# Kernel tuning notes

Hardware: AMD Instinct MI355X
Metric: run time of the kernel (lower is better)

## Reference

```python
import jax, jax.numpy as jnp
import numpy as np

EPS = 1e-6

def _silu(x):
    return x * jax.nn.sigmoid(x)

def setup_inputs() -> dict:
    key = jax.random.key(0)
    ks = jax.random.split(key, 6)
    T, B, D, N = 2048, 16, 1024, 64
    scale = (6.0 / (N + D)) ** 0.5  # xavier_uniform bound
    x = jax.random.normal(ks[0], (T, B, D), dtype=jnp.float32)
    S0 = jnp.zeros((B, N, N), dtype=jnp.float32)
    W_k = jax.random.uniform(ks[1], (N, D), minval=-scale, maxval=scale, dtype=jnp.float32)
    W_v = jax.random.uniform(ks[2], (N, D), minval=-scale, maxval=scale, dtype=jnp.float32)
    W_q = jax.random.uniform(ks[3], (N, D), minval=-scale, maxval=scale, dtype=jnp.float32)
    W_beta = jax.random.uniform(ks[4], (N, D), minval=-scale, maxval=scale, dtype=jnp.float32)
    b_beta = jnp.full((N,), 2.0, dtype=jnp.float32)
    return {"x": x, "S0": S0, "W_k": W_k, "W_v": W_v, "W_q": W_q, "W_beta": W_beta, "b_beta": b_beta}

def reference(x, S0, W_k, W_v, W_q, W_beta, b_beta):
    # x: [T, B, D] -> projections [T, B, n]
    k_all = jnp.einsum('tbd,nd->tbn', x, W_k)
    v_all = jnp.einsum('tbd,nd->tbn', x, W_v)
    q_all = jnp.einsum('tbd,nd->tbn', x, W_q)
    beta_all = jax.nn.sigmoid(jnp.einsum('tbd,nd->tbn', x, W_beta) + b_beta)

    def step(S, inp):
        k, v, q, beta = inp  # each [B, n]
        k_norm = k / (jnp.linalg.norm(k, axis=-1, keepdims=True) + EPS)
        retrieved = jnp.einsum('bij,bj->bi', S, k_norm)
        delta = v - retrieved
        outer = jnp.einsum('bi,bj->bij', delta, k_norm)
        S_new = jnp.tanh(beta[:, :, None] * S + outer)
        Sq = jnp.einsum('bij,bj->bi', S_new, q)
        out = Sq * _silu(Sq)
        return S_new, out

    S_final, output = jax.lax.scan(step, S0, (k_all, v_all, q_all, beta_all))
    return output, S_final
```

## Files before the change

### kernel.cpp

```cpp
#include <hip/hip_runtime.h>
#include <math.h>
#include <stdint.h>

#define T_DIM 2048
#define B_DIM 16
#define D_DIM 1024
#define N_DIM 64
#define EPSV 1e-6f

#define NT 256

#define TWO_LOG2E 2.885390081777927f
#define LOG2E     1.4426950408889634f

typedef _Float16 half8 __attribute__((ext_vector_type(8)));
typedef float    f32x16_t __attribute__((ext_vector_type(16)));
union F4H8 { float4 f; half8 h; };

__device__ __forceinline__ float fast_rcp(float x) {
    return __builtin_amdgcn_rcpf(x);
}
__device__ __forceinline__ float sigmoid_fast(float x) {
    return fast_rcp(1.f + __builtin_amdgcn_exp2f(-LOG2E * x));
}
__device__ __forceinline__ float tanh_from_scaled(float xs) {
    float e = __builtin_amdgcn_exp2f(xs);
    return 1.f - 2.f * fast_rcp(e + 1.f);
}

template<int CTRL>
__device__ __forceinline__ float dpp_radd(float x) {
    int y = __builtin_amdgcn_update_dpp(0, __float_as_int(x), CTRL, 0xf, 0xf, true);
    return x + __int_as_float(y);
}
__device__ __forceinline__ float reduce16(float x) {
    x = dpp_radd<0xB1>(x);
    x = dpp_radd<0x4E>(x);
    x = dpp_radd<0x124>(x);
    x = dpp_radd<0x128>(x);
    return x;
}

__device__ __forceinline__ void dma16(const float* g, float* l) {
    __builtin_amdgcn_global_load_lds((const __attribute__((address_space(1))) void*)g,
                                     (__attribute__((address_space(3))) void*)l, 16, 0, 0);
}

__global__ __launch_bounds__(256) void wprep_kernel(
    const float* __restrict__ Wk, const float* __restrict__ Wv,
    const float* __restrict__ Wq, const float* __restrict__ Wb,
    float4* __restrict__ w2)
{
    const int c  = threadIdx.x;
    const int k8 = blockIdx.x;
    const float* Wsrc = (c < 64) ? Wk : (c < 128) ? Wv : (c < 192) ? Wq : Wb;
    const float4* src = (const float4*)(Wsrc + (size_t)(c & 63) * D_DIM + k8 * 8);
    const float4 f0 = src[0], f1 = src[1];
    float f[8] = {f0.x, f0.y, f0.z, f0.w, f1.x, f1.y, f1.z, f1.w};
    F4H8 hi, lo;
    #pragma unroll
    for (int j = 0; j < 8; ++j) {
        _Float16 h = (_Float16)f[j];
        hi.h[j] = h;
        lo.h[j] = (_Float16)(f[j] - (float)h);
    }
    w2[(size_t)(2 * k8)     * 256 + c] = hi.f;
    w2[(size_t)(2 * k8 + 1) * 256 + c] = lo.f;
}

#define BM 64

__global__ __launch_bounds__(256) void proj_gemm_mfma(
    const float* __restrict__ x,
    const float4* __restrict__ w2,
    const float* __restrict__ bb,
    float* __restrict__ proj)
{
    __shared__ float  As32[2][BM * 32];
    __shared__ float4 Ahl[2][BM * 8];

    const int tid  = threadIdx.x;
    const int w    = tid >> 6;
    const int lane = tid & 63;
    const int m0   = blockIdx.x * BM;
    const int cl   = lane & 31;
    const int kh   = lane >> 5;

    f32x16_t acc[2][2] = {};

    auto stage = [&](int buf, int t) {
        #pragma unroll
        for (int i = 0; i < 2; ++i) {
            const int rb    = w * 16 + i * 8;
            const int row   = rb + (lane >> 3);
            const int sslot = (lane & 7) ^ ((lane >> 3) & 7);
            dma16(x + (size_t)(m0 + row) * D_DIM + 32 * t + 4 * sslot,
                  &As32[buf][rb * 32]);
        }
    };
    auto convert = [&](int bs, int bd) {
        const int row = tid >> 2, c = tid & 3, sw = row & 7;
        const float4* s32 = (const float4*)&As32[bs][0];
        const float4 fA = s32[row * 8 + ((2 * c)     ^ sw)];
        const float4 fB = s32[row * 8 + ((2 * c + 1) ^ sw)];
        float f[8] = {fA.x, fA.y, fA.z, fA.w, fB.x, fB.y, fB.z, fB.w};
        F4H8 hi, lo;
        #pragma unroll
        for (int j = 0; j < 8; ++j) {
            _Float16 h = (_Float16)f[j];
            hi.h[j] = h;
            lo.h[j] = (_Float16)(f[j] - (float)h);
        }
        Ahl[bd][row * 8 + ((2 * c)     ^ sw)] = hi.f;
        Ahl[bd][row * 8 + ((2 * c + 1) ^ sw)] = lo.f;
    };

    stage(0, 0);
    stage(1, 1);
    __syncthreads();
    convert(0, 0);
    __syncthreads();

    for (int t = 0; t < 32; ++t) {
        if (t + 2 < 32) stage(t & 1, t + 2);

        half8 bh[2][2], bl[2][2];
        #pragma unroll
        for (int ks = 0; ks < 2; ++ks) {
            const int ksg = 2 * t + ks;
            #pragma unroll
            for (int tn = 0; tn < 2; ++tn) {
                const int col = w * 64 + tn * 32 + cl;
                F4H8 th, tl;
                th.f = w2[(size_t)(4 * ksg + 2 * kh)     * 256 + col];
                tl.f = w2[(size_t)(4 * ksg + 2 * kh + 1) * 256 + col];
                bh[ks][tn] = th.h; bl[ks][tn] = tl.h;
            }
        }

        if (t + 1 < 32) convert((t + 1) & 1, (t + 1) & 1);

        const float4* At = &Ahl[t & 1][0];
        #pragma unroll
        for (int ks = 0; ks < 2; ++ks) {
            half8 ah[2], al[2];
            #pragma unroll
            for (int tm = 0; tm < 2; ++tm) {
                const int row = tm * 32 + cl;
                const int sw  = row & 7;
                F4H8 th, tl;
                th.f = At[row * 8 + ((4 * ks + 2 * kh)     ^ sw)];
                tl.f = At[row * 8 + ((4 * ks + 2 * kh + 1) ^ sw)];
                ah[tm] = th.h; al[tm] = tl.h;
            }
            #pragma unroll
            for (int tm = 0; tm < 2; ++tm)
                #pragma unroll
                for (int tn = 0; tn < 2; ++tn) {
                    acc[tm][tn] = __builtin_amdgcn_mfma_f32_32x32x16_f16(ah[tm], bh[ks][tn], acc[tm][tn], 0, 0, 0);
                    acc[tm][tn] = __builtin_amdgcn_mfma_f32_32x32x16_f16(ah[tm], bl[ks][tn], acc[tm][tn], 0, 0, 0);
                    acc[tm][tn] = __builtin_amdgcn_mfma_f32_32x32x16_f16(al[tm], bh[ks][tn], acc[tm][tn], 0, 0, 0);
                }
        }
        __syncthreads();
    }

    #pragma unroll
    for (int tn = 0; tn < 2; ++tn) {
        const int  gcol   = w * 64 + tn * 32 + cl;
        const bool isbeta = (gcol >= 192);
        const float bias  = isbeta ? bb[gcol - 192] : 0.f;
        #pragma unroll
        for (int tm = 0; tm < 2; ++tm) {
            #pragma unroll
            for (int r = 0; r < 16; ++r) {
                const int rowin = (r & 3) + 8 * (r >> 2) + 4 * kh;
                const size_t grow = (size_t)(m0 + tm * 32 + rowin);
                float v = acc[tm][tn][r];
                if (isbeta) v = sigmoid_fast(v + bias);
                proj[grow * NT + gcol] = v;
            }
        }
    }
}

__global__ __launch_bounds__(256) void knorm_kernel(float* __restrict__ proj)
{
    const int w = (int)((blockIdx.x * blockDim.x + threadIdx.x) >> 6);
    const int lane = threadIdx.x & 63;
    float k = proj[(size_t)w * NT + lane];
    float s = k * k;
    #pragma unroll
    for (int off = 32; off; off >>= 1) s += __shfl_xor(s, off, 64);
    proj[(size_t)w * NT + lane] = k * fast_rcp(sqrtf(s) + EPSV);
}

__device__ __forceinline__ void step_body(float4& s, const float4 kn, const float4 q,
                                          const float vC, const float beC,
                                          int sp, int l, float& ysel)
{
    float y2 = (s.x * kn.x + s.y * kn.y) + (s.z * kn.z + s.w * kn.w);
    y2 = reduce16(y2);
    const float dC = fmaf(-TWO_LOG2E, y2, vC);
    const float bsx = beC * s.x, bsy = beC * s.y;
    const float bsz = beC * s.z, bsw = beC * s.w;
    s.x = tanh_from_scaled(fmaf(dC, kn.x, bsx));
    s.y = tanh_from_scaled(fmaf(dC, kn.y, bsy));
    s.z = tanh_from_scaled(fmaf(dC, kn.z, bsz));
    s.w = tanh_from_scaled(fmaf(dC, kn.w, bsw));
    float y1 = (s.x * q.x + s.y * q.y) + (s.z * q.z + s.w * q.w);
    y1 = reduce16(y1);
    ysel = (l == sp) ? y1 : ysel;
}

__device__ __forceinline__ void phase16(const float (*buf)[256], int t0,
                                        float4& s, int l, int i, int b,
                                        float* __restrict__ out)
{
    const float* s0 = &buf[0][0];
    const float* s1 = &buf[1][0];
    float4 kn0 = *(const float4*)(s0 + 4 * l);
    float4 q0  = *(const float4*)(s0 + 128 + 4 * l);
    float  vC0 = s0[64 + i] * TWO_LOG2E;
    float  beC0= s0[192 + i] * TWO_LOG2E;
    float4 kn1 = *(const float4*)(s1 + 4 * l);
    float4 q1  = *(const float4*)(s1 + 128 + 4 * l);
    float  vC1 = s1[64 + i] * TWO_LOG2E;
    float  beC1= s1[192 + i] * TWO_LOG2E;

    float ysel = 0.f;
    for (int j = 0; j < 8; ++j) {
        const int sp = 2 * j;
        const int p2 = (sp + 2 < 16) ? sp + 2 : 15;
        const int p3 = (sp + 3 < 16) ? sp + 3 : 15;
        const float* sA = &buf[p2][0];
        const float* sB = &buf[p3][0];
        float4 knA = *(const float4*)(sA + 4 * l);
        float4 qA  = *(const float4*)(sA + 128 + 4 * l);
        float  vCA = sA[64 + i] * TWO_LOG2E;
        float  beCA= sA[192 + i] * TWO_LOG2E;
        float4 knB = *(const float4*)(sB + 4 * l);
        float4 qB  = *(const float4*)(sB + 128 + 4 * l);
        float  vCB = sB[64 + i] * TWO_LOG2E;
        float  beCB= sB[192 + i] * TWO_LOG2E;

        step_body(s, kn0, q0, vC0, beC0, sp,     l, ysel);
        step_body(s, kn1, q1, vC1, beC1, sp + 1, l, ysel);

        kn0 = knA; q0 = qA; vC0 = vCA; beC0 = beCA;
        kn1 = knB; q1 = qB; vC1 = vCB; beC1 = beCB;
    }
    const float w = ysel;
    out[(size_t)(t0 + l) * (B_DIM * N_DIM) + b * 64 + i] = w * w * sigmoid_fast(w);
}

__global__ __launch_bounds__(128, 1) void recur6_kernel(
    const float* __restrict__ proj,
    const float* __restrict__ S0,
    float* __restrict__ out)
{
    __shared__ float bufA[16][256];
    __shared__ float bufB[16][256];

    const int wid  = blockIdx.x;
    const int wv   = threadIdx.x >> 6;
    const int lane = threadIdx.x & 63;
    const int l = lane & 15;
    const int r = lane >> 4;
    const int b = wid >> 4;
    const int i = ((wid & 15) << 2) + r;

    if (wv == 1) {
        #pragma unroll
        for (int j = 0; j < 16; ++j)
            dma16(proj + ((size_t)j * B_DIM + b) * NT + 4 * lane, &bufA[j][0]);
        __syncthreads();
        for (int t0 = 0; t0 < T_DIM; t0 += 32) {
            #pragma unroll
            for (int j = 0; j < 16; ++j) {
                int row = t0 + 16 + j; if (row > T_DIM - 1) row = T_DIM - 1;
                dma16(proj + ((size_t)row * B_DIM + b) * NT + 4 * lane, &bufB[j][0]);
            }
            __syncthreads();
            #pragma unroll
            for (int j = 0; j < 16; ++j) {
                int row = t0 + 32 + j; if (row > T_DIM - 1) row = T_DIM - 1;
                dma16(proj + ((size_t)row * B_DIM + b) * NT + 4 * lane, &bufA[j][0]);
            }
            __syncthreads();
        }
    } else {
        float4 s = *(const float4*)(S0 + ((size_t)(b * 64 + i) << 6) + 4 * l);
        __syncthreads();
        for (int t0 = 0; t0 < T_DIM; t0 += 32) {
            phase16(bufA, t0, s, l, i, b, out);
            __syncthreads();
            phase16(bufB, t0 + 16, s, l, i, b, out);
            __syncthreads();
        }
        *(float4*)(out + (size_t)T_DIM * B_DIM * N_DIM +
                   ((size_t)(b * 64 + i) << 6) + 4 * l) = s;
    }
}

extern "C" void kernel_launch(void* const* d_in, const int* in_sizes, int n_in,
                              void* d_out, int out_size, void* d_ws, size_t ws_size,
                              hipStream_t stream) {
    const float* x  = (const float*)d_in[0];
    const float* S0 = (const float*)d_in[1];
    const float* Wk = (const float*)d_in[2];
    const float* Wv = (const float*)d_in[3];
    const float* Wq = (const float*)d_in[4];
    const float* Wb = (const float*)d_in[5];
    const float* bb = (const float*)d_in[6];
    float* out  = (float*)d_out;
    float* proj = (float*)d_ws;
    float4* w2  = (float4*)((char*)d_ws + (size_t)32768 * 256 * 4);

    wprep_kernel<<<dim3(128), dim3(256), 0, stream>>>(Wk, Wv, Wq, Wb, w2);
    proj_gemm_mfma<<<dim3(32768 / BM), dim3(256), 0, stream>>>(x, w2, bb, proj);
    knorm_kernel<<<dim3((32768 * 64) / 256), dim3(256), 0, stream>>>(proj);
    recur6_kernel<<<dim3(256), dim3(128), 0, stream>>>(proj, S0, out);
}
```

Before: 470.1 us.

## Interleave output reduction with next step's state reduction and raise compute wave priority

Each recurrence step's q-projection reduction is deferred and run interleaved with the next step's S·k reduction using DPP row-add operations, so the two serial cross-lane reductions share latency. The tanh argument is algebraically split so the v/beta terms are computed before the reduction finishes. The final step's output is reduced after the loop, and the compute wave gets a higher scheduling priority than the DMA wave. This adds register pressure and depends on the dpp_radd helpers being correct for 16-lane groups.

```diff
diff --git a/kernel.cpp b/kernel.cpp
--- a/kernel.cpp
+++ b/kernel.cpp
@@ -195,22 +195,28 @@
     proj[(size_t)w * NT + lane] = k * fast_rcp(sqrtf(s) + EPSV);
 }
 
-__device__ __forceinline__ void step_body(float4& s, const float4 kn, const float4 q,
-                                          const float vC, const float beC,
-                                          int sp, int l, float& ysel)
-{
-    float y2 = (s.x * kn.x + s.y * kn.y) + (s.z * kn.z + s.w * kn.w);
-    y2 = reduce16(y2);
-    const float dC = fmaf(-TWO_LOG2E, y2, vC);
-    const float bsx = beC * s.x, bsy = beC * s.y;
-    const float bsz = beC * s.z, bsw = beC * s.w;
-    s.x = tanh_from_scaled(fmaf(dC, kn.x, bsx));
-    s.y = tanh_from_scaled(fmaf(dC, kn.y, bsy));
-    s.z = tanh_from_scaled(fmaf(dC, kn.z, bsz));
-    s.w = tanh_from_scaled(fmaf(dC, kn.w, bsw));
-    float y1 = (s.x * q.x + s.y * q.y) + (s.z * q.z + s.w * q.w);
-    y1 = reduce16(y1);
-    ysel = (l == sp) ? y1 : ysel;
+__device__ __forceinline__ void step_rot(float4& s, const float4 kn, const float4 q,
+                                         const float vC, const float beC,
+                                         const int cap, const int l,
+                                         float& ysel, float& p1)
+{
+    float p2 = (s.x * kn.x + s.y * kn.y) + (s.z * kn.z + s.w * kn.w);
+    const float Px = fmaf(vC, kn.x, beC * s.x);
+    const float Py = fmaf(vC, kn.y, beC * s.y);
+    const float Pz = fmaf(vC, kn.z, beC * s.z);
+    const float Pw = fmaf(vC, kn.w, beC * s.w);
+    const float Qx = TWO_LOG2E * kn.x, Qy = TWO_LOG2E * kn.y;
+    const float Qz = TWO_LOG2E * kn.z, Qw = TWO_LOG2E * kn.w;
+    p2 = dpp_radd<0xB1>(p2);   p1 = dpp_radd<0xB1>(p1);
+    p2 = dpp_radd<0x4E>(p2);   p1 = dpp_radd<0x4E>(p1);
+    p2 = dpp_radd<0x124>(p2);  p1 = dpp_radd<0x124>(p1);
+    p2 = dpp_radd<0x128>(p2);  p1 = dpp_radd<0x128>(p1);
+    ysel = (l == cap) ? p1 : ysel;
+    s.x = tanh_from_scaled(fmaf(-Qx, p2, Px));
+    s.y = tanh_from_scaled(fmaf(-Qy, p2, Py));
+    s.z = tanh_from_scaled(fmaf(-Qz, p2, Pz));
+    s.w = tanh_from_scaled(fmaf(-Qw, p2, Pw));
+    p1 = (s.x * q.x + s.y * q.y) + (s.z * q.z + s.w * q.w);
 }
 
 __device__ __forceinline__ void phase16(const float (*buf)[256], int t0,
@@ -228,13 +234,13 @@
     float  vC1 = s1[64 + i] * TWO_LOG2E;
     float  beC1= s1[192 + i] * TWO_LOG2E;
 
-    float ysel = 0.f;
+    float ysel = 0.f, p1 = 0.f;
     for (int j = 0; j < 8; ++j) {
         const int sp = 2 * j;
-        const int p2 = (sp + 2 < 16) ? sp + 2 : 15;
-        const int p3 = (sp + 3 < 16) ? sp + 3 : 15;
-        const float* sA = &buf[p2][0];
-        const float* sB = &buf[p3][0];
+        const int pA = (sp + 2 < 16) ? sp + 2 : 15;
+        const int pB = (sp + 3 < 16) ? sp + 3 : 15;
+        const float* sA = &buf[pA][0];
+        const float* sB = &buf[pB][0];
         float4 knA = *(const float4*)(sA + 4 * l);
         float4 qA  = *(const float4*)(sA + 128 + 4 * l);
         float  vCA = sA[64 + i] * TWO_LOG2E;
@@ -244,12 +250,14 @@
         float  vCB = sB[64 + i] * TWO_LOG2E;
         float  beCB= sB[192 + i] * TWO_LOG2E;
 
-        step_body(s, kn0, q0, vC0, beC0, sp,     l, ysel);
-        step_body(s, kn1, q1, vC1, beC1, sp + 1, l, ysel);
+        step_rot(s, kn0, q0, vC0, beC0, sp - 1, l, ysel, p1);
+        step_rot(s, kn1, q1, vC1, beC1, sp,     l, ysel, p1);
 
         kn0 = knA; q0 = qA; vC0 = vCA; beC0 = beCA;
         kn1 = knB; q1 = qB; vC1 = vCB; beC1 = beCB;
     }
+    p1 = reduce16(p1);
+    ysel = (l == 15) ? p1 : ysel;
     const float w = ysel;
     out[(size_t)(t0 + l) * (B_DIM * N_DIM) + b * 64 + i] = w * w * sigmoid_fast(w);
 }
@@ -290,6 +298,7 @@
             __syncthreads();
         }
     } else {
+        __builtin_amdgcn_s_setprio(1);
         float4 s = *(const float4*)(S0 + ((size_t)(b * 64 + i) << 6) + 4 * l);
         __syncthreads();
         for (int t0 = 0; t0 < T_DIM; t0 += 32) {
```

Result: slower. 533.3 us (+13.5%).

## Map one state row per wave with full 64-lane reductions in recurrence

Applied to the files above, without the earlier changes.

Restructures the recurrence kernel so each of four compute waves owns one state row, with each lane holding a single state element, instead of one wave handling four rows with float4 per lane. Dot products now use a full 64-lane DPP reduction plus readlane, and the tanh update is folded algebraically into one exp2 argument. Outputs are buffered over 64 steps and written once per 64 timesteps. The aim is to cut per-lane serial work on the latency-bound recurrence by using more waves per block, at the cost of longer cross-row reductions and a larger block.

```diff
diff --git a/kernel.cpp b/kernel.cpp
--- a/kernel.cpp
+++ b/kernel.cpp
@@ -23,22 +23,21 @@
 __device__ __forceinline__ float sigmoid_fast(float x) {
     return fast_rcp(1.f + __builtin_amdgcn_exp2f(-LOG2E * x));
 }
-__device__ __forceinline__ float tanh_from_scaled(float xs) {
-    float e = __builtin_amdgcn_exp2f(xs);
-    return 1.f - 2.f * fast_rcp(e + 1.f);
-}
 
 template<int CTRL>
 __device__ __forceinline__ float dpp_radd(float x) {
     int y = __builtin_amdgcn_update_dpp(0, __float_as_int(x), CTRL, 0xf, 0xf, true);
     return x + __int_as_float(y);
 }
-__device__ __forceinline__ float reduce16(float x) {
+
+__device__ __forceinline__ float reduce64_rl(float x) {
     x = dpp_radd<0xB1>(x);
     x = dpp_radd<0x4E>(x);
     x = dpp_radd<0x124>(x);
     x = dpp_radd<0x128>(x);
-    return x;
+    x = dpp_radd<0x142>(x);
+    x = dpp_radd<0x143>(x);
+    return __int_as_float(__builtin_amdgcn_readlane(__float_as_int(x), 63));
 }
 
 __device__ __forceinline__ void dma16(const float* g, float* l) {
@@ -195,66 +194,48 @@
     proj[(size_t)w * NT + lane] = k * fast_rcp(sqrtf(s) + EPSV);
 }
 
-__device__ __forceinline__ void step_body(float4& s, const float4 kn, const float4 q,
-                                          const float vC, const float beC,
-                                          int sp, int l, float& ysel)
-{
-    float y2 = (s.x * kn.x + s.y * kn.y) + (s.z * kn.z + s.w * kn.w);
-    y2 = reduce16(y2);
-    const float dC = fmaf(-TWO_LOG2E, y2, vC);
-    const float bsx = beC * s.x, bsy = beC * s.y;
-    const float bsz = beC * s.z, bsw = beC * s.w;
-    s.x = tanh_from_scaled(fmaf(dC, kn.x, bsx));
-    s.y = tanh_from_scaled(fmaf(dC, kn.y, bsy));
-    s.z = tanh_from_scaled(fmaf(dC, kn.z, bsz));
-    s.w = tanh_from_scaled(fmaf(dC, kn.w, bsw));
-    float y1 = (s.x * q.x + s.y * q.y) + (s.z * q.z + s.w * q.w);
-    y1 = reduce16(y1);
-    ysel = (l == sp) ? y1 : ysel;
-}
-
-__device__ __forceinline__ void phase16(const float (*buf)[256], int t0,
-                                        float4& s, int l, int i, int b,
-                                        float* __restrict__ out)
-{
-    const float* s0 = &buf[0][0];
-    const float* s1 = &buf[1][0];
-    float4 kn0 = *(const float4*)(s0 + 4 * l);
-    float4 q0  = *(const float4*)(s0 + 128 + 4 * l);
-    float  vC0 = s0[64 + i] * TWO_LOG2E;
-    float  beC0= s0[192 + i] * TWO_LOG2E;
-    float4 kn1 = *(const float4*)(s1 + 4 * l);
-    float4 q1  = *(const float4*)(s1 + 128 + 4 * l);
-    float  vC1 = s1[64 + i] * TWO_LOG2E;
-    float  beC1= s1[192 + i] * TWO_LOG2E;
-
-    float ysel = 0.f;
+__device__ __forceinline__ void step_r7(float& s, const float kn, const float q,
+                                        const float Q2, const float vC, const float beC,
+                                        const int cap, const int lane, float& ysel)
+{
+    float y2 = reduce64_rl(s * kn);
+    float P  = fmaf(vC, kn, beC * s);
+    float e  = __builtin_amdgcn_exp2f(fmaf(-Q2, y2, P));
+    s = fmaf(-2.f, fast_rcp(e + 1.f), 1.f);
+    float y1 = reduce64_rl(s * q);
+    ysel = (lane == cap) ? y1 : ysel;
+}
+
+__device__ __forceinline__ void phase16_r7(const float (*buf)[256], int t0,
+                                           float& s, int lane, int i, float& ysel)
+{
+    const float* r0 = &buf[0][0];
+    const float* r1 = &buf[1][0];
+    float kn0 = r0[lane], q0 = r0[128 + lane];
+    float vC0 = r0[64 + i] * TWO_LOG2E, beC0 = r0[192 + i] * TWO_LOG2E;
+    float kn1 = r1[lane], q1 = r1[128 + lane];
+    float vC1 = r1[64 + i] * TWO_LOG2E, beC1 = r1[192 + i] * TWO_LOG2E;
+
     for (int j = 0; j < 8; ++j) {
         const int sp = 2 * j;
-        const int p2 = (sp + 2 < 16) ? sp + 2 : 15;
-        const int p3 = (sp + 3 < 16) ? sp + 3 : 15;
-        const float* sA = &buf[p2][0];
-        const float* sB = &buf[p3][0];
-        float4 knA = *(const float4*)(sA + 4 * l);
-        float4 qA  = *(const float4*)(sA + 128 + 4 * l);
-        float  vCA = sA[64 + i] * TWO_LOG2E;
-        float  beCA= sA[192 + i] * TWO_LOG2E;
-        float4 knB = *(const float4*)(sB + 4 * l);
-        float4 qB  = *(const float4*)(sB + 128 + 4 * l);
-        float  vCB = sB[64 + i] * TWO_LOG2E;
-        float  beCB= sB[192 + i] * TWO_LOG2E;
-
-        step_body(s, kn0, q0, vC0, beC0, sp,     l, ysel);
-        step_body(s, kn1, q1, vC1, beC1, sp + 1, l, ysel);
+        const int pA = (sp + 2 < 16) ? sp + 2 : 15;
+        const int pB = (sp + 3 < 16) ? sp + 3 : 15;
+        const float* rA = &buf[pA][0];
+        const float* rB = &buf[pB][0];
+        float knA = rA[lane], qA = rA[128 + lane];
+        float vCA = rA[64 + i] * TWO_LOG2E, beCA = rA[192 + i] * TWO_LOG2E;
+        float knB = rB[lane], qB = rB[128 + lane];
+        float vCB = rB[64 + i] * TWO_LOG2E, beCB = rB[192 + i] * TWO_LOG2E;
+
+        step_r7(s, kn0, q0, TWO_LOG2E * kn0, vC0, beC0, (t0 + sp) & 63,     lane, ysel);
+        step_r7(s, kn1, q1, TWO_LOG2E * kn1, vC1, beC1, (t0 + sp + 1) & 63, lane, ysel);
 
         kn0 = knA; q0 = qA; vC0 = vCA; beC0 = beCA;
         kn1 = knB; q1 = qB; vC1 = vCB; beC1 = beCB;
     }
-    const float w = ysel;
-    out[(size_t)(t0 + l) * (B_DIM * N_DIM) + b * 64 + i] = w * w * sigmoid_fast(w);
-}
-
-__global__ __launch_bounds__(128, 1) void recur6_kernel(
+}
+
+__global__ __launch_bounds__(320, 1) void recur7_kernel(
     const float* __restrict__ proj,
     const float* __restrict__ S0,
     float* __restrict__ out)
@@ -265,12 +246,10 @@
     const int wid  = blockIdx.x;
     const int wv   = threadIdx.x >> 6;
     const int lane = threadIdx.x & 63;
-    const int l = lane & 15;
-    const int r = lane >> 4;
     const int b = wid >> 4;
-    const int i = ((wid & 15) << 2) + r;
-
-    if (wv == 1) {
+    const int i = ((wid & 15) << 2) + wv;
+
+    if (wv == 4) {
         #pragma unroll
         for (int j = 0; j < 16; ++j)
             dma16(proj + ((size_t)j * B_DIM + b) * NT + 4 * lane, &bufA[j][0]);
@@ -290,16 +269,21 @@
             __syncthreads();
         }
     } else {
-        float4 s = *(const float4*)(S0 + ((size_t)(b * 64 + i) << 6) + 4 * l);
+        float s = S0[((size_t)(b * 64 + i) << 6) + lane];
+        float ysel = 0.f;
         __syncthreads();
         for (int t0 = 0; t0 < T_DIM; t0 += 32) {
-            phase16(bufA, t0, s, l, i, b, out);
+            phase16_r7(bufA, t0, s, lane, i, ysel);
             __syncthreads();
-            phase16(bufB, t0 + 16, s, l, i, b, out);
+            phase16_r7(bufB, t0 + 16, s, lane, i, ysel);
+            if ((t0 & 63) == 32) {
+                const float w = ysel;
+                out[(size_t)(t0 - 32 + lane) * (B_DIM * N_DIM) + b * 64 + i] =
+                    w * w * sigmoid_fast(w);
+            }
             __syncthreads();
         }
-        *(float4*)(out + (size_t)T_DIM * B_DIM * N_DIM +
-                   ((size_t)(b * 64 + i) << 6) + 4 * l) = s;
+        out[(size_t)T_DIM * B_DIM * N_DIM + ((size_t)(b * 64 + i) << 6) + lane] = s;
     }
 }
 
@@ -320,5 +304,5 @@
     wprep_kernel<<<dim3(128), dim3(256), 0, stream>>>(Wk, Wv, Wq, Wb, w2);
     proj_gemm_mfma<<<dim3(32768 / BM), dim3(256), 0, stream>>>(x, w2, bb, proj);
     knorm_kernel<<<dim3((32768 * 64) / 256), dim3(256), 0, stream>>>(proj);
-    recur6_kernel<<<dim3(256), dim3(128), 0, stream>>>(proj, S0, out);
-}
+    recur7_kernel<<<dim3(256), dim3(320), 0, stream>>>(proj, S0, out);
+}
```

After: 501.2 us. 6.6% more time.

## Split recurrence into serial state wave and separate output wave via LDS ring

Applied to the files above, without the earlier changes.

The recurrence kernel gains a third wavefront. One wave now runs only the serial state update and writes each step's state into a double-buffered LDS ring. A second wave computes the Sq readout and SiLU output for the previous 16-step phase from that ring, with q loaded from global memory. The loader wave pre-scales v and beta by 2*log2(e) in LDS, and the serial wave is given higher priority. This takes the q dot-product reduction off the critical serial path, at the cost of extra LDS traffic and a third wave competing for issue slots.

```diff
diff --git a/kernel.cpp b/kernel.cpp
--- a/kernel.cpp
+++ b/kernel.cpp
@@ -25,7 +25,7 @@
 }
 __device__ __forceinline__ float tanh_from_scaled(float xs) {
     float e = __builtin_amdgcn_exp2f(xs);
-    return 1.f - 2.f * fast_rcp(e + 1.f);
+    return fmaf(-2.f, fast_rcp(e + 1.f), 1.f);
 }
 
 template<int CTRL>
@@ -195,72 +195,80 @@
     proj[(size_t)w * NT + lane] = k * fast_rcp(sqrtf(s) + EPSV);
 }
 
-__device__ __forceinline__ void step_body(float4& s, const float4 kn, const float4 q,
-                                          const float vC, const float beC,
-                                          int sp, int l, float& ysel)
+__device__ __forceinline__ void step_ser(float4& s, const float4 kn,
+                                         const float vC, const float beC,
+                                         float* __restrict__ ring_dst)
 {
     float y2 = (s.x * kn.x + s.y * kn.y) + (s.z * kn.z + s.w * kn.w);
     y2 = reduce16(y2);
-    const float dC = fmaf(-TWO_LOG2E, y2, vC);
+    const float a = fmaf(-TWO_LOG2E, y2, vC);
     const float bsx = beC * s.x, bsy = beC * s.y;
     const float bsz = beC * s.z, bsw = beC * s.w;
-    s.x = tanh_from_scaled(fmaf(dC, kn.x, bsx));
-    s.y = tanh_from_scaled(fmaf(dC, kn.y, bsy));
-    s.z = tanh_from_scaled(fmaf(dC, kn.z, bsz));
-    s.w = tanh_from_scaled(fmaf(dC, kn.w, bsw));
-    float y1 = (s.x * q.x + s.y * q.y) + (s.z * q.z + s.w * q.w);
-    y1 = reduce16(y1);
-    ysel = (l == sp) ? y1 : ysel;
-}
-
-__device__ __forceinline__ void phase16(const float (*buf)[256], int t0,
-                                        float4& s, int l, int i, int b,
-                                        float* __restrict__ out)
+    s.x = tanh_from_scaled(fmaf(a, kn.x, bsx));
+    s.y = tanh_from_scaled(fmaf(a, kn.y, bsy));
+    s.z = tanh_from_scaled(fmaf(a, kn.z, bsz));
+    s.w = tanh_from_scaled(fmaf(a, kn.w, bsw));
+    *(float4*)ring_dst = s;
+}
+
+__device__ __forceinline__ void phase_ser(const float (*buf)[256],
+                                          float (*ring)[4][64],
+                                          float4& s, int l, int r, int i)
 {
     const float* s0 = &buf[0][0];
     const float* s1 = &buf[1][0];
     float4 kn0 = *(const float4*)(s0 + 4 * l);
-    float4 q0  = *(const float4*)(s0 + 128 + 4 * l);
-    float  vC0 = s0[64 + i] * TWO_LOG2E;
-    float  beC0= s0[192 + i] * TWO_LOG2E;
+    float  vC0 = s0[64 + i], beC0 = s0[192 + i];
     float4 kn1 = *(const float4*)(s1 + 4 * l);
-    float4 q1  = *(const float4*)(s1 + 128 + 4 * l);
-    float  vC1 = s1[64 + i] * TWO_LOG2E;
-    float  beC1= s1[192 + i] * TWO_LOG2E;
-
-    float ysel = 0.f;
+    float  vC1 = s1[64 + i], beC1 = s1[192 + i];
+
     for (int j = 0; j < 8; ++j) {
         const int sp = 2 * j;
-        const int p2 = (sp + 2 < 16) ? sp + 2 : 15;
-        const int p3 = (sp + 3 < 16) ? sp + 3 : 15;
-        const float* sA = &buf[p2][0];
-        const float* sB = &buf[p3][0];
+        const int pA = (sp + 2 < 16) ? sp + 2 : 15;
+        const int pB = (sp + 3 < 16) ? sp + 3 : 15;
+        const float* sA = &buf[pA][0];
+        const float* sB = &buf[pB][0];
         float4 knA = *(const float4*)(sA + 4 * l);
-        float4 qA  = *(const float4*)(sA + 128 + 4 * l);
-        float  vCA = sA[64 + i] * TWO_LOG2E;
-        float  beCA= sA[192 + i] * TWO_LOG2E;
+        float  vCA = sA[64 + i], beCA = sA[192 + i];
         float4 knB = *(const float4*)(sB + 4 * l);
-        float4 qB  = *(const float4*)(sB + 128 + 4 * l);
-        float  vCB = sB[64 + i] * TWO_LOG2E;
-        float  beCB= sB[192 + i] * TWO_LOG2E;
-
-        step_body(s, kn0, q0, vC0, beC0, sp,     l, ysel);
-        step_body(s, kn1, q1, vC1, beC1, sp + 1, l, ysel);
-
-        kn0 = knA; q0 = qA; vC0 = vCA; beC0 = beCA;
-        kn1 = knB; q1 = qB; vC1 = vCB; beC1 = beCB;
+        float  vCB = sB[64 + i], beCB = sB[192 + i];
+
+        step_ser(s, kn0, vC0, beC0, &ring[sp][r][4 * l]);
+        step_ser(s, kn1, vC1, beC1, &ring[sp + 1][r][4 * l]);
+
+        kn0 = knA; vC0 = vCA; beC0 = beCA;
+        kn1 = knB; vC1 = vCB; beC1 = beCB;
+    }
+}
+
+__device__ __forceinline__ void phase_y1(const float (*ring)[4][64],
+                                         const float* __restrict__ proj,
+                                         int t0, int b, int l, int r, int i,
+                                         float* __restrict__ out)
+{
+    float4 q[16];
+    #pragma unroll
+    for (int sp = 0; sp < 16; ++sp)
+        q[sp] = *(const float4*)(proj + ((size_t)(t0 + sp) * B_DIM + b) * NT + 128 + 4 * l);
+    float ysel = 0.f;
+    #pragma unroll
+    for (int sp = 0; sp < 16; ++sp) {
+        const float4 sv = *(const float4*)(&ring[sp][r][4 * l]);
+        float y1 = (sv.x * q[sp].x + sv.y * q[sp].y) + (sv.z * q[sp].z + sv.w * q[sp].w);
+        y1 = reduce16(y1);
+        ysel = (l == sp) ? y1 : ysel;
     }
     const float w = ysel;
     out[(size_t)(t0 + l) * (B_DIM * N_DIM) + b * 64 + i] = w * w * sigmoid_fast(w);
 }
 
-__global__ __launch_bounds__(128, 1) void recur6_kernel(
+__global__ __launch_bounds__(192, 1) void recur8_kernel(
     const float* __restrict__ proj,
     const float* __restrict__ S0,
     float* __restrict__ out)
 {
-    __shared__ float bufA[16][256];
-    __shared__ float bufB[16][256];
+    __shared__ float buf[2][16][256];
+    __shared__ float ring[2][16][4][64];
 
     const int wid  = blockIdx.x;
     const int wv   = threadIdx.x >> 6;
@@ -270,36 +278,44 @@
     const int b = wid >> 4;
     const int i = ((wid & 15) << 2) + r;
 
-    if (wv == 1) {
-        #pragma unroll
-        for (int j = 0; j < 16; ++j)
-            dma16(proj + ((size_t)j * B_DIM + b) * NT + 4 * lane, &bufA[j][0]);
+    if (wv == 2) {
+        auto fill = [&](int pb, int tfirst) {
+            #pragma unroll
+            for (int j = 0; j < 16; ++j) {
+                int row = tfirst + j; if (row > T_DIM - 1) row = T_DIM - 1;
+                dma16(proj + ((size_t)row * B_DIM + b) * NT + 4 * lane, &buf[pb][j][0]);
+            }
+            asm volatile("s_waitcnt vmcnt(0)");
+            #pragma unroll
+            for (int j = 0; j < 16; ++j) {
+                buf[pb][j][64 + lane]  *= TWO_LOG2E;
+                buf[pb][j][192 + lane] *= TWO_LOG2E;
+            }
+        };
+        fill(0, 0);
         __syncthreads();
-        for (int t0 = 0; t0 < T_DIM; t0 += 32) {
-            #pragma unroll
-            for (int j = 0; j < 16; ++j) {
-                int row = t0 + 16 + j; if (row > T_DIM - 1) row = T_DIM - 1;
-                dma16(proj + ((size_t)row * B_DIM + b) * NT + 4 * lane, &bufB[j][0]);
-            }
+        for (int p = 0; p < 128; ++p) {
+            fill((p + 1) & 1, 16 * (p + 1));
             __syncthreads();
-            #pragma unroll
-            for (int j = 0; j < 16; ++j) {
-                int row = t0 + 32 + j; if (row > T_DIM - 1) row = T_DIM - 1;
-                dma16(proj + ((size_t)row * B_DIM + b) * NT + 4 * lane, &bufA[j][0]);
-            }
-            __syncthreads();
-        }
-    } else {
+        }
+    } else if (wv == 0) {
+        __builtin_amdgcn_s_setprio(1);
         float4 s = *(const float4*)(S0 + ((size_t)(b * 64 + i) << 6) + 4 * l);
         __syncthreads();
-        for (int t0 = 0; t0 < T_DIM; t0 += 32) {
-            phase16(bufA, t0, s, l, i, b, out);
-            __syncthreads();
-            phase16(bufB, t0 + 16, s, l, i, b, out);
+        for (int p = 0; p < 128; ++p) {
+            phase_ser(buf[p & 1], ring[p & 1], s, l, r, i);
             __syncthreads();
         }
         *(float4*)(out + (size_t)T_DIM * B_DIM * N_DIM +
                    ((size_t)(b * 64 + i) << 6) + 4 * l) = s;
+    } else {
+        __syncthreads();
+        for (int p = 0; p < 128; ++p) {
+            if (p >= 1)
+                phase_y1(ring[(p - 1) & 1], proj, 16 * (p - 1), b, l, r, i, out);
+            __syncthreads();
+        }
+        phase_y1(ring[1], proj, 16 * 127, b, l, r, i, out);
     }
 }
 
@@ -320,5 +336,5 @@
     wprep_kernel<<<dim3(128), dim3(256), 0, stream>>>(Wk, Wv, Wq, Wb, w2);
     proj_gemm_mfma<<<dim3(32768 / BM), dim3(256), 0, stream>>>(x, w2, bb, proj);
     knorm_kernel<<<dim3((32768 * 64) / 256), dim3(256), 0, stream>>>(proj);
-    recur6_kernel<<<dim3(256), dim3(128), 0, stream>>>(proj, S0, out);
-}
+    recur8_kernel<<<dim3(256), dim3(192), 0, stream>>>(proj, S0, out);
+}
```

Result: no change. 470.6 us (+0.1%).
